# Performance work log

Hardware: AMD Instinct MI355X
Metric: run time of the kernel (lower is better)

The kernel has to match this reference:

```python
import jax, jax.numpy as jnp
import numpy as np

N, G, D, A = 131072, 256, 256, 64
NEG = -1e9
EPS = 1e-10


def segment_softmax(logits, idx, num_segments):
    # numerically stable softmax over ragged segments; works for [N] and [N, A]
    m = jax.ops.segment_max(logits, idx, num_segments=num_segments)
    e = jnp.exp(logits - m[idx])
    s = jax.ops.segment_sum(e, idx, num_segments=num_segments)
    return e / s[idx]


def setup_inputs() -> dict:
    key = jax.random.key(0)
    ks = jax.random.split(key, 12)
    values = jax.random.normal(ks[0], (N, D), dtype=jnp.float32)
    indices = jnp.sort(jax.random.randint(ks[1], (N,), 0, G))
    a_action = jax.random.randint(ks[2], (G,), 0, A)
    a_node = jax.random.randint(ks[3], (G,), 0, N)
    action_mask = jax.random.randint(ks[4], (G, A), 0, 2).astype(bool)
    n_nodes = jax.ops.segment_sum(jnp.ones((N,), jnp.int32), indices, num_segments=G)
    s = 0.02
    w_node = jax.random.normal(ks[5], (D,), dtype=jnp.float32) * s          # node_prob (no bias)
    W_agn = jax.random.normal(ks[6], (A, D), dtype=jnp.float32) * s         # action_given_node_prob
    b_agn = jnp.zeros((A,), jnp.float32)
    W_nga = jax.random.normal(ks[7], (A, D), dtype=jnp.float32) * s         # node_given_action_prob
    b_nga = jnp.zeros((A,), jnp.float32)
    W_qna = jax.random.normal(ks[8], (A, D), dtype=jnp.float32) * s         # q_node__action
    b_qna = jnp.zeros((A,), jnp.float32)
    W_qan = jax.random.normal(ks[9], (A, D), dtype=jnp.float32) * s         # q_action__node
    b_qan = jnp.zeros((A,), jnp.float32)
    return {"values": values, "indices": indices, "a_action": a_action, "a_node": a_node,
            "action_mask": action_mask, "n_nodes": n_nodes,
            "w_node": w_node, "W_agn": W_agn, "b_agn": b_agn, "W_nga": W_nga, "b_nga": b_nga,
            "W_qna": W_qna, "b_qna": b_qna, "W_qan": W_qan, "b_qan": b_qan}


def reference(values, indices, a_action, a_node, action_mask, n_nodes,
              w_node, W_agn, b_agn, W_nga, b_nga, W_qna, b_qna, W_qan, b_qan):
    n_g = action_mask.shape[0]
    segsum = lambda x: jax.ops.segment_sum(x, indices, num_segments=n_g)

    node_logits = values @ w_node                         # [N]
    agn_logits = values @ W_agn.T + b_agn                 # [N, A] action_given_node
    nga_logits = values @ W_nga.T + b_nga                 # [N, A] node_given_action
    mask_actions = action_mask[indices]                   # [N, A] per-node action validity

    # p(n) per graph, p(a|n) per node, p(a) per graph by marginalization
    p_n = segment_softmax(node_logits, indices, n_g)                       # [N]
    p_a_given_n = jax.nn.softmax(jnp.where(mask_actions, agn_logits, NEG), axis=-1)  # [N, A]
    p_a = segsum(p_n[:, None] * p_a_given_n)                               # [G, A]

    # masked p(n|a) used for eval (logprob/entropy)
    p_n_a_masked = segment_softmax(jnp.where(mask_actions, nga_logits, NEG), indices, n_g)  # [N, A]

    g_ar = jnp.arange(n_g)
    logprob = jnp.log(p_a[g_ar, a_action] + EPS) + jnp.log(p_n_a_masked[a_node, a_action] + EPS)  # [G]

    H_a = -jnp.sum(p_a * jnp.log(p_a + EPS), axis=-1)                      # [G]
    H_n_given_a = -segsum(p_n_a_masked * jnp.log(p_n_a_masked + EPS))      # [G, A]
    entropy = H_a + jnp.sum(p_a * H_n_given_a, axis=-1)                    # [G]

    # value estimate (unmasked p_n__a, as in f())
    p_n__a = segment_softmax(nga_logits, indices, n_g)                     # [N, A]
    q_a = segsum(values @ W_qan.T + b_qan)                                 # [G, A]
    q_n__a = values @ W_qna.T + b_qna                                      # [N, A]
    value = jnp.sum(p_a * (q_a + segsum(p_n__a * q_n__a)), axis=-1)        # [G]

    return (logprob, entropy, value, p_a, p_n__a)
```

## Files before the change

### kernel.cpp

```cpp
#include <hip/hip_runtime.h>
#include <hip/hip_bf16.h>

typedef unsigned short u16;
typedef unsigned int u32;
typedef __attribute__((ext_vector_type(4))) float f32x4;
typedef __attribute__((ext_vector_type(8))) short s16x8;
typedef __attribute__((ext_vector_type(8))) unsigned short u16x8;
typedef __attribute__((ext_vector_type(4))) unsigned short u16x4;

#define EPS_V (1e-10f)
#define TILES 4
#define NHALF (TILES * 4)

__device__ __forceinline__ u16 f2bf(float f) {
  unsigned u = __float_as_uint(f);
  u += 0x7fffu + ((u >> 16) & 1u);
  return (u16)(u >> 16);
}
__device__ __forceinline__ float bf2f(u16 h) {
  return __uint_as_float(((unsigned)h) << 16);
}
__device__ __forceinline__ float wred_sum(float v) {
#pragma unroll
  for (int o = 32; o; o >>= 1) v += __shfl_xor(v, o);
  return v;
}
__device__ __forceinline__ bool mask_at(const void* m, int kind, int idx) {
  if (kind == 0) return ((const int*)m)[idx] != 0;
  if (kind == 1) return ((const float*)m)[idx] != 0.0f;
  return ((const unsigned char*)m)[idx] != 0;
}

__global__ __launch_bounds__(256) void k0_fused(
    const int* __restrict__ n_nodes, const unsigned int* __restrict__ mask_raw,
    const float* __restrict__ w_node, const float* __restrict__ W_agn,
    const float* __restrict__ W_nga, const float* __restrict__ W_qna,
    const float* __restrict__ W_qan,
    int* __restrict__ seg_start, int* __restrict__ mkind,
    float* __restrict__ q_a, u16* __restrict__ Wpack, int G, int ndw) {
  const int b = blockIdx.x;
  const int t = threadIdx.x;
  if (b == 0) {
    if (t < 64) {
      int base = t * 4;
      int v0 = (base + 0 < G) ? n_nodes[base + 0] : 0;
      int v1 = (base + 1 < G) ? n_nodes[base + 1] : 0;
      int v2 = (base + 2 < G) ? n_nodes[base + 2] : 0;
      int v3 = (base + 3 < G) ? n_nodes[base + 3] : 0;
      int lsum = v0 + v1 + v2 + v3;
      int x = lsum;
#pragma unroll
      for (int o = 1; o < 64; o <<= 1) {
        int y = __shfl_up(x, o);
        if (t >= o) x += y;
      }
      int run = x - lsum;
      if (base + 0 < G) seg_start[base + 0] = run; run += v0;
      if (base + 1 < G) seg_start[base + 1] = run; run += v1;
      if (base + 2 < G) seg_start[base + 2] = run; run += v2;
      if (base + 3 < G) seg_start[base + 3] = run; run += v3;
      if (t == 63) seg_start[G] = run;
    }
  } else if (b == 1) {
    __shared__ int notInt, notFloat;
    if (t == 0) { notInt = 0; notFloat = 0; }
    __syncthreads();
    int li = 0, lf = 0;
    for (int i = t; i < ndw; i += 256) {
      unsigned v = mask_raw[i];
      if (v != 0u && v != 1u) li = 1;
      if (v != 0u && v != 0x3F800000u) lf = 1;
    }
    if (li) atomicOr(&notInt, 1);
    if (lf) atomicOr(&notFloat, 1);
    __syncthreads();
    if (t == 0) mkind[0] = (!notInt) ? 0 : ((!notFloat) ? 1 : 2);
  } else if (b < 2 + 80) {
    int q = (b - 2) * 256 + t;
    int col = q >> 6, k = (q & 63) * 4;
    f32x4 v = (f32x4){0.f, 0.f, 0.f, 0.f};
    if (col < 64) v = *reinterpret_cast<const f32x4*>(W_agn + col * 256 + k);
    else if (col < 128) v = *reinterpret_cast<const f32x4*>(W_nga + (col - 64) * 256 + k);
    else if (col < 192) v = *reinterpret_cast<const f32x4*>(W_qna + (col - 128) * 256 + k);
    else if (col < 256) v = *reinterpret_cast<const f32x4*>(W_qan + (col - 192) * 256 + k);
    else if (col == 256) v = *reinterpret_cast<const f32x4*>(w_node + k);
    u16x4 h;
    h[0] = f2bf(v[0]); h[1] = f2bf(v[1]); h[2] = f2bf(v[2]); h[3] = f2bf(v[3]);
    *reinterpret_cast<u16x4*>(Wpack + (size_t)q * 4) = h;
  } else {
    int idx = (b - 82) * 256 + t;
    if (idx < G * 64) q_a[idx] = 0.f;
  }
}

__device__ __forceinline__ s16x8 frag_from_lds(const float* Vf, int m, int k0) {
  int g0 = ((k0 >> 2) ^ (m & 7));
  int g1 = g0 ^ 1;
  const f32x4 lo = *reinterpret_cast<const f32x4*>(&Vf[m * 256 + g0 * 4]);
  const f32x4 hi = *reinterpret_cast<const f32x4*>(&Vf[m * 256 + g1 * 4]);
  union { s16x8 v; u32 u[4]; } r;
  r.u[0] = __builtin_amdgcn_perm(__float_as_uint(lo[1]), __float_as_uint(lo[0]), 0x07060302u);
  r.u[1] = __builtin_amdgcn_perm(__float_as_uint(lo[3]), __float_as_uint(lo[2]), 0x07060302u);
  r.u[2] = __builtin_amdgcn_perm(__float_as_uint(hi[1]), __float_as_uint(hi[0]), 0x07060302u);
  r.u[3] = __builtin_amdgcn_perm(__float_as_uint(hi[3]), __float_as_uint(hi[2]), 0x07060302u);
  return r.v;
}

__global__ __launch_bounds__(256, 2) void k1_gemm(
    const float* __restrict__ values, const u16* __restrict__ Wpack,
    const int* __restrict__ indices,
    const float* __restrict__ b_agn, const float* __restrict__ b_nga,
    const float* __restrict__ b_qna, const float* __restrict__ b_qan,
    u16* __restrict__ agn, u16* __restrict__ nga_bf, float* __restrict__ nga_f32,
    u16* __restrict__ qna, float* __restrict__ q_a,
    float* __restrict__ nl, int nga_is_bf) {
  __shared__ float ring[4][16 * 256];
  __shared__ u16 outbuf[3][16][68];
  __shared__ float nlbuf[16];
  __shared__ int segid[TILES * 64];

  const int t = threadIdx.x;
  const int lane = t & 63;
  const int wave = t >> 6;
  const int ln15 = lane & 15;
  const int kg = lane >> 4;
  const int blk0 = blockIdx.x * (TILES * 64);

  s16x8 bfr[4][8];
  {
    const u16* wb = Wpack + (size_t)(wave * 64 + ln15) * 256 + kg * 8;
#pragma unroll
    for (int cg = 0; cg < 4; ++cg)
#pragma unroll
      for (int s = 0; s < 8; ++s)
        bfr[cg][s] = *reinterpret_cast<const s16x8*>(wb + (size_t)(cg * 16) * 256 + s * 32);
  }
  float bias_c[4];
  {
    const float* bp = (wave == 0) ? b_agn : (wave == 1) ? b_nga
                    : (wave == 2) ? b_qna : b_qan;
#pragma unroll
    for (int cg = 0; cg < 4; ++cg) bias_c[cg] = bp[cg * 16 + ln15];
  }
  s16x8 bn[8];
  if (wave == 0) {
    const u16* wb = Wpack + (size_t)(256 + ln15) * 256 + kg * 8;
#pragma unroll
    for (int s = 0; s < 8; ++s)
      bn[s] = *reinterpret_cast<const s16x8*>(wb + s * 32);
  }
  if (wave == 3) {
#pragma unroll
    for (int j = 0; j < 4; ++j)
      segid[lane + 64 * j] = indices[blk0 + lane + 64 * j];
  }
  float qpart[4] = {0.f, 0.f, 0.f, 0.f};
  int qg = (wave == 3) ? segid[kg * 4] : 0;

#define STAGE(hh)                                                              \
  {                                                                            \
    float* dst_ = ring[(hh) & 3];                                              \
    const int r0_ = blk0 + (hh) * 16;                                          \
    _Pragma("unroll")                                                          \
    for (int i_ = 0; i_ < 4; ++i_) {                                           \
      int m_ = wave * 4 + i_;                                                  \
      const float* gp_ = values + (size_t)(r0_ + m_) * 256 + ((lane ^ (m_ & 7)) << 2); \
      __builtin_amdgcn_global_load_lds(                                        \
          (const __attribute__((address_space(1))) void*)gp_,                  \
          (__attribute__((address_space(3))) void*)&dst_[m_ * 256], 16, 0, 0); \
    }                                                                          \
  }

  STAGE(0);
  STAGE(1);

  for (int h = 0; h < NHALF; ++h) {
    if (h + 2 < NHALF) STAGE(h + 2);
    if (!nga_is_bf && wave == 1) {
      asm volatile("s_waitcnt vmcnt(0)" ::: "memory");
    } else if (h == 0) {
      asm volatile("s_waitcnt vmcnt(8)" ::: "memory");
    } else if (h == NHALF - 1) {
      asm volatile("s_waitcnt vmcnt(0)" ::: "memory");
    } else if (h == NHALF - 2) {
      if (wave == 0)      asm volatile("s_waitcnt vmcnt(9)" ::: "memory");
      else if (wave == 3) asm volatile("s_waitcnt vmcnt(4)" ::: "memory");
      else                asm volatile("s_waitcnt vmcnt(8)" ::: "memory");
    } else {
      if (wave == 0)      asm volatile("s_waitcnt vmcnt(13)" ::: "memory");
      else if (wave == 3) asm volatile("s_waitcnt vmcnt(8)" ::: "memory");
      else                asm volatile("s_waitcnt vmcnt(12)" ::: "memory");
    }
    __builtin_amdgcn_sched_barrier(0);
    __builtin_amdgcn_s_barrier();
    __builtin_amdgcn_sched_barrier(0);

    const float* buf = ring[h & 3];
    const int row0 = blk0 + h * 16;

    f32x4 acc[4];
#pragma unroll
    for (int cg = 0; cg < 4; ++cg) acc[cg] = (f32x4){0.f, 0.f, 0.f, 0.f};
    f32x4 an0 = (f32x4){0.f, 0.f, 0.f, 0.f};

#pragma unroll
    for (int s = 0; s < 8; ++s) {
      const int k0 = s * 32 + kg * 8;
      s16x8 a0 = frag_from_lds(buf, ln15, k0);
#pragma unroll
      for (int cg = 0; cg < 4; ++cg)
        acc[cg] = __builtin_amdgcn_mfma_f32_16x16x32_bf16(a0, bfr[cg][s], acc[cg], 0, 0, 0);
      if (wave == 0)
        an0 = __builtin_amdgcn_mfma_f32_16x16x32_bf16(a0, bn[s], an0, 0, 0, 0);
    }

    if (wave == 3) {
#pragma unroll
      for (int r = 0; r < 4; ++r) {
        int m = kg * 4 + r;
        int g = segid[h * 16 + m];
        if (g != qg) {
#pragma unroll
          for (int cg = 0; cg < 4; ++cg) {
            atomicAdd(&q_a[qg * 64 + cg * 16 + ln15], qpart[cg]);
            qpart[cg] = 0.f;
          }
          qg = g;
        }
#pragma unroll
        for (int cg = 0; cg < 4; ++cg)
          qpart[cg] += acc[cg][r] + bias_c[cg];
      }
    } else if (wave == 1 && !nga_is_bf) {
#pragma unroll
      for (int r = 0; r < 4; ++r)
#pragma unroll
        for (int cg = 0; cg < 4; ++cg)
          nga_f32[(size_t)(row0 + kg * 4 + r) * 64 + cg * 16 + ln15] = acc[cg][r] + bias_c[cg];
    } else {
#pragma unroll
      for (int r = 0; r < 4; ++r) {
        int m = kg * 4 + r;
#pragma unroll
        for (int cg = 0; cg < 4; ++cg)
          outbuf[wave][m][cg * 16 + ln15] = f2bf(acc[cg][r] + bias_c[cg]);
      }
      if (wave == 0 && ln15 == 0) {
#pragma unroll
        for (int r = 0; r < 4; ++r) nlbuf[kg * 4 + r] = an0[r];
      }
      u16* dstp = (wave == 0) ? agn : (wave == 1) ? nga_bf : qna;
#pragma unroll
      for (int j = 0; j < 4; ++j) {
        int li = lane + j * 64;
        int rr = li >> 4, cc = (li & 15) * 4;
        u16x4 v = *reinterpret_cast<const u16x4*>(&outbuf[wave][rr][cc]);
        *reinterpret_cast<u16x4*>(dstp + (size_t)row0 * 64 + (size_t)li * 4) = v;
      }
      if (wave == 0 && lane < 16) nl[row0 + lane] = nlbuf[lane];
    }
  }
#undef STAGE

  if (wave == 3) {
#pragma unroll
    for (int cg = 0; cg < 4; ++cg)
      atomicAdd(&q_a[qg * 64 + cg * 16 + ln15], qpart[cg]);
  }
}

__global__ __launch_bounds__(1024) void k2_segment(
    const u16* __restrict__ agn, const u16* __restrict__ nga_bf,
    float* __restrict__ nga_f32, const u16* __restrict__ qna,
    const float* __restrict__ nl, const int* __restrict__ seg_start,
    const void* __restrict__ mask, const int* __restrict__ mkind,
    const float* __restrict__ q_a,
    float* __restrict__ p_a, float* __restrict__ entropy, float* __restrict__ value,
    float* __restrict__ Su, float* __restrict__ pna, int nga_is_bf) {
  const int g = blockIdx.x;
  const int s = seg_start[g], e = seg_start[g + 1];
  const int n = e - s;
  const int t = threadIdx.x, lane = t & 63, wave = t >> 6;

  __shared__ float wbuf[16];
  __shared__ float cs[16][64], cv[16][64], ci[16][64], cp[16][64];
  __shared__ float sS[64];

  float ls = 0.f;
  for (int i = s + t; i < e; i += 1024) ls += __expf(nl[i]);
  ls = wred_sum(ls);
  if (lane == 0) wbuf[wave] = ls;
  __syncthreads();
  float Sn = 0.f;
#pragma unroll
  for (int w = 0; w < 16; ++w) Sn += wbuf[w];
  float invSn = (Sn > 0.f) ? 1.f / Sn : 0.f;

  const int kind = mkind[0];
  const bool mv = mask_at(mask, kind, g * 64 + lane);
  float s_u = 0.f, v_u = 0.f, i_u = 0.f, pa = 0.f;
  for (int i = s + wave; i < e; i += 16) {
    size_t base = (size_t)i * 64 + lane;
    float pn = __expf(nl[i]) * invSn;
    float ev = mv ? __expf(bf2f(agn[base])) : 0.f;
    float rs = wred_sum(ev);
    pa += pn * ((rs > 0.f) ? ev / rs : 0.015625f);
    float y = nga_is_bf ? bf2f(nga_bf[base]) : nga_f32[base];
    float ey = __expf(y);
    s_u += ey;
    v_u += ey * y;
    i_u += ey * bf2f(qna[base]);
  }
  cs[wave][lane] = s_u; cv[wave][lane] = v_u; ci[wave][lane] = i_u;
  cp[wave][lane] = pa;
  __syncthreads();

  if (t < 64) {
    int a = t;
    float S = 0.f, V = 0.f, I = 0.f, P = 0.f;
#pragma unroll
    for (int w = 0; w < 16; ++w) {
      S += cs[w][a]; V += cv[w][a]; I += ci[w][a]; P += cp[w][a];
    }
    p_a[g * 64 + a] = P;
    Su[g * 64 + a] = S;
    sS[a] = (S > 0.f) ? 1.f / S : 0.f;
    float inner = (S > 0.f) ? I / S : 0.f;
    float Q = q_a[g * 64 + a];
    bool mva = mask_at(mask, kind, g * 64 + a);
    float Hn;
    if (n <= 0) Hn = 0.f;
    else if (!mva) Hn = -logf(1.0f / (float)n + EPS_V);
    else Hn = (S > 0.f) ? (logf(S) - V / S) : 0.f;
    float ent_c = -P * logf(P + EPS_V) + P * Hn;
    float val_c = P * (Q + inner);
    ent_c = wred_sum(ent_c);
    val_c = wred_sum(val_c);
    if (a == 0) { entropy[g] = ent_c; value[g] = val_c; }
  }
  __syncthreads();

  const int a0 = (t & 7) * 8;
  float is0 = sS[a0 + 0], is1 = sS[a0 + 1], is2 = sS[a0 + 2], is3 = sS[a0 + 3];
  float is4 = sS[a0 + 4], is5 = sS[a0 + 5], is6 = sS[a0 + 6], is7 = sS[a0 + 7];
  for (int i = s + (t >> 3); i < e; i += 128) {
    size_t base = (size_t)i * 64 + a0;
    float4 o0, o1;
    if (nga_is_bf) {
      u16x8 y = *reinterpret_cast<const u16x8*>(nga_bf + base);
      o0.x = __expf(bf2f(y[0])) * is0; o0.y = __expf(bf2f(y[1])) * is1;
      o0.z = __expf(bf2f(y[2])) * is2; o0.w = __expf(bf2f(y[3])) * is3;
      o1.x = __expf(bf2f(y[4])) * is4; o1.y = __expf(bf2f(y[5])) * is5;
      o1.z = __expf(bf2f(y[6])) * is6; o1.w = __expf(bf2f(y[7])) * is7;
    } else {
      const float4* src = reinterpret_cast<const float4*>(nga_f32 + base);
      float4 x0 = src[0], x1 = src[1];
      o0.x = __expf(x0.x) * is0; o0.y = __expf(x0.y) * is1;
      o0.z = __expf(x0.z) * is2; o0.w = __expf(x0.w) * is3;
      o1.x = __expf(x1.x) * is4; o1.y = __expf(x1.y) * is5;
      o1.z = __expf(x1.z) * is6; o1.w = __expf(x1.w) * is7;
    }
    float4* dst = reinterpret_cast<float4*>(pna + base);
    dst[0] = o0; dst[1] = o1;
  }
}

__global__ __launch_bounds__(256) void k3_logprob(
    const float* __restrict__ p_a, const u16* __restrict__ nga_bf,
    const float* __restrict__ nga_f32, const int* __restrict__ indices,
    const int* __restrict__ a_action, const int* __restrict__ a_node,
    const void* __restrict__ mask, const int* __restrict__ mkind,
    const int* __restrict__ n_nodes, const float* __restrict__ Su,
    float* __restrict__ logprob, int G, int nga_is_bf) {
  int g = blockIdx.x * blockDim.x + threadIdx.x;
  if (g >= G) return;
  int kind = mkind[0];
  int a = a_action[g];
  float t1 = logf(p_a[g * 64 + a] + EPS_V);
  int node = a_node[g];
  int g2 = indices[node];
  float p2;
  if (mask_at(mask, kind, g2 * 64 + a)) {
    float S = Su[g2 * 64 + a];
    float y = nga_is_bf ? bf2f(nga_bf[(size_t)node * 64 + a]) : nga_f32[(size_t)node * 64 + a];
    p2 = (S > 0.f) ? __expf(y) / S : 0.f;
  } else {
    p2 = 1.0f / (float)n_nodes[g2];
  }
  logprob[g] = t1 + logf(p2 + EPS_V);
}

extern "C" void kernel_launch(void* const* d_in, const int* in_sizes, int n_in,
                              void* d_out, int out_size, void* d_ws, size_t ws_size,
                              hipStream_t stream) {
  const float* values = (const float*)d_in[0];
  const int* indices = (const int*)d_in[1];
  const int* a_action = (const int*)d_in[2];
  const int* a_node = (const int*)d_in[3];
  const void* action_mask = d_in[4];
  const int* n_nodes = (const int*)d_in[5];
  const float* w_node = (const float*)d_in[6];
  const float* W_agn = (const float*)d_in[7];
  const float* b_agn = (const float*)d_in[8];
  const float* W_nga = (const float*)d_in[9];
  const float* b_nga = (const float*)d_in[10];
  const float* W_qna = (const float*)d_in[11];
  const float* b_qna = (const float*)d_in[12];
  const float* W_qan = (const float*)d_in[13];
  const float* b_qan = (const float*)d_in[14];

  const int N = in_sizes[1];
  const int G = in_sizes[2];
  const int GA = in_sizes[4];

  float* out = (float*)d_out;
  float* o_logprob = out;
  float* o_entropy = out + G;
  float* o_value = out + 2 * G;
  float* o_pa = out + 3 * G;
  float* o_pna = out + 3 * G + GA;

  char* w = (char*)d_ws;
  size_t off = 0;
  u16* agn = (u16*)(w + off); off += (size_t)N * 64 * 2;
  u16* qna = (u16*)(w + off); off += (size_t)N * 64 * 2;
  float* nl = (float*)(w + off); off += (size_t)N * 4;
  float* Su = (float*)(w + off); off += (size_t)GA * 4;
  float* q_a = (float*)(w + off); off += (size_t)GA * 4;
  int* seg_start = (int*)(w + off); off += (size_t)(G + 1) * 4;
  int* mkind = (int*)(w + off); off += 256;
  off = (off + 255) & ~(size_t)255;
  u16* Wpack = (u16*)(w + off); off += (size_t)320 * 256 * 2;
  u16* nga_bf = (u16*)(w + off);
  size_t need_bf = off + (size_t)N * 64 * 2;
  int nga_is_bf = (ws_size >= need_bf) ? 1 : 0;
  float* nga_f32 = o_pna;

  int zero_blocks = (GA + 255) / 256;
  k0_fused<<<2 + 80 + zero_blocks, 256, 0, stream>>>(
      n_nodes, (const unsigned int*)action_mask, w_node, W_agn, W_nga, W_qna, W_qan,
      seg_start, mkind, q_a, Wpack, G, GA / 4);
  k1_gemm<<<N / (TILES * 64), 256, 0, stream>>>(
      values, Wpack, indices, b_agn, b_nga, b_qna, b_qan,
      agn, nga_bf, nga_f32, qna, q_a, nl, nga_is_bf);
  k2_segment<<<G, 1024, 0, stream>>>(agn, nga_bf, nga_f32, qna, nl, seg_start,
                                     action_mask, mkind, q_a,
                                     o_pa, o_entropy, o_value, Su, o_pna, nga_is_bf);
  k3_logprob<<<(G + 255) / 256, 256, 0, stream>>>(
      o_pa, nga_bf, nga_f32, indices, a_action, a_node,
      action_mask, mkind, n_nodes, Su, o_logprob, G, nga_is_bf);
}
```

Measured before the change: 95.87 us.

## Fuse action-given-node softmax and p_a accumulation into GEMM epilogue

The GEMM kernel now computes the masked per-row softmax of the action-given-node logits, along with the exponentiated node logits, directly in wave 0's epilogue. It accumulates unnormalized p_a and the node-softmax denominator per segment with atomics, so the bf16 agn and nl intermediates are no longer written to or reread from global memory. The segment kernel then only normalizes p_a by the accumulated denominator. This removes about 16MB of intermediate traffic and a reduction pass. The cost is extra exp and shuffle work plus atomics in the GEMM. Node logits are also exponentiated without max subtraction, which relies on them being small.

Measured after the change: 95.52 us (median of 2 runs). About the same (-0.4%).

```diff
diff --git a/kernel.cpp b/kernel.cpp
--- a/kernel.cpp
+++ b/kernel.cpp
@@ -25,6 +25,11 @@
   for (int o = 32; o; o >>= 1) v += __shfl_xor(v, o);
   return v;
 }
+__device__ __forceinline__ float red16(float v) {
+  v += __shfl_xor(v, 1); v += __shfl_xor(v, 2);
+  v += __shfl_xor(v, 4); v += __shfl_xor(v, 8);
+  return v;
+}
 __device__ __forceinline__ bool mask_at(const void* m, int kind, int idx) {
   if (kind == 0) return ((const int*)m)[idx] != 0;
   if (kind == 1) return ((const float*)m)[idx] != 0.0f;
@@ -37,7 +42,8 @@
     const float* __restrict__ W_nga, const float* __restrict__ W_qna,
     const float* __restrict__ W_qan,
     int* __restrict__ seg_start, int* __restrict__ mkind,
-    float* __restrict__ q_a, u16* __restrict__ Wpack, int G, int ndw) {
+    float* __restrict__ zero_base, int nzero, u16* __restrict__ Wpack,
+    int G, int ndw) {
   const int b = blockIdx.x;
   const int t = threadIdx.x;
   if (b == 0) {
@@ -89,7 +95,7 @@
     *reinterpret_cast<u16x4*>(Wpack + (size_t)q * 4) = h;
   } else {
     int idx = (b - 82) * 256 + t;
-    if (idx < G * 64) q_a[idx] = 0.f;
+    if (idx < nzero) zero_base[idx] = 0.f;
   }
 }
 
@@ -108,15 +114,15 @@
 
 __global__ __launch_bounds__(256, 2) void k1_gemm(
     const float* __restrict__ values, const u16* __restrict__ Wpack,
-    const int* __restrict__ indices,
+    const int* __restrict__ indices, const void* __restrict__ mask,
+    const int* __restrict__ mkind,
     const float* __restrict__ b_agn, const float* __restrict__ b_nga,
     const float* __restrict__ b_qna, const float* __restrict__ b_qan,
-    u16* __restrict__ agn, u16* __restrict__ nga_bf, float* __restrict__ nga_f32,
+    u16* __restrict__ nga_bf, float* __restrict__ nga_f32,
     u16* __restrict__ qna, float* __restrict__ q_a,
-    float* __restrict__ nl, int nga_is_bf) {
+    float* __restrict__ pa_un, float* __restrict__ Sn_at, int nga_is_bf) {
   __shared__ float ring[4][16 * 256];
-  __shared__ u16 outbuf[3][16][68];
-  __shared__ float nlbuf[16];
+  __shared__ u16 outbuf[2][16][68];
   __shared__ int segid[TILES * 64];
 
   const int t = threadIdx.x;
@@ -125,6 +131,7 @@
   const int ln15 = lane & 15;
   const int kg = lane >> 4;
   const int blk0 = blockIdx.x * (TILES * 64);
+  const int kind = mkind[0];
 
   s16x8 bfr[4][8];
   {
@@ -156,6 +163,16 @@
   }
   float qpart[4] = {0.f, 0.f, 0.f, 0.f};
   int qg = (wave == 3) ? segid[kg * 4] : 0;
+  float pa_[4] = {0.f, 0.f, 0.f, 0.f};
+  float sn_ = 0.f;
+  int pg = 0;
+  bool mv[4] = {false, false, false, false};
+  if (wave == 0) {
+    pg = indices[blk0 + kg * 4];
+#pragma unroll
+    for (int cg = 0; cg < 4; ++cg)
+      mv[cg] = mask_at(mask, kind, pg * 64 + cg * 16 + ln15);
+  }
 
 #define STAGE(hh)                                                              \
   {                                                                            \
@@ -176,20 +193,18 @@
 
   for (int h = 0; h < NHALF; ++h) {
     if (h + 2 < NHALF) STAGE(h + 2);
-    if (!nga_is_bf && wave == 1) {
+    if (h == 0) {
+      asm volatile("s_waitcnt vmcnt(8) lgkmcnt(0)" ::: "memory");
+    } else if (!nga_is_bf && wave == 1) {
       asm volatile("s_waitcnt vmcnt(0)" ::: "memory");
-    } else if (h == 0) {
-      asm volatile("s_waitcnt vmcnt(8)" ::: "memory");
     } else if (h == NHALF - 1) {
       asm volatile("s_waitcnt vmcnt(0)" ::: "memory");
     } else if (h == NHALF - 2) {
-      if (wave == 0)      asm volatile("s_waitcnt vmcnt(9)" ::: "memory");
-      else if (wave == 3) asm volatile("s_waitcnt vmcnt(4)" ::: "memory");
-      else                asm volatile("s_waitcnt vmcnt(8)" ::: "memory");
+      if (wave == 1 || wave == 2) asm volatile("s_waitcnt vmcnt(8)" ::: "memory");
+      else                        asm volatile("s_waitcnt vmcnt(4)" ::: "memory");
     } else {
-      if (wave == 0)      asm volatile("s_waitcnt vmcnt(13)" ::: "memory");
-      else if (wave == 3) asm volatile("s_waitcnt vmcnt(8)" ::: "memory");
-      else                asm volatile("s_waitcnt vmcnt(12)" ::: "memory");
+      if (wave == 1 || wave == 2) asm volatile("s_waitcnt vmcnt(12)" ::: "memory");
+      else                        asm volatile("s_waitcnt vmcnt(8)" ::: "memory");
     }
     __builtin_amdgcn_sched_barrier(0);
     __builtin_amdgcn_s_barrier();
@@ -214,7 +229,44 @@
         an0 = __builtin_amdgcn_mfma_f32_16x16x32_bf16(a0, bn[s], an0, 0, 0, 0);
     }
 
-    if (wave == 3) {
+    if (wave == 0) {
+#pragma unroll
+      for (int r = 0; r < 4; ++r) {
+        int m = kg * 4 + r;
+        int g = segid[h * 16 + m];
+        if (g != pg) {
+#pragma unroll
+          for (int cg = 0; cg < 4; ++cg) {
+            atomicAdd(&pa_un[pg * 64 + cg * 16 + ln15], pa_[cg]);
+            pa_[cg] = 0.f;
+          }
+          if (ln15 == 0) atomicAdd(&Sn_at[pg], sn_);
+          sn_ = 0.f;
+          pg = g;
+#pragma unroll
+          for (int cg = 0; cg < 4; ++cg)
+            mv[cg] = mask_at(mask, kind, pg * 64 + cg * 16 + ln15);
+        }
+        float e0[4];
+        float rs = 0.f;
+#pragma unroll
+        for (int cg = 0; cg < 4; ++cg) {
+          e0[cg] = mv[cg] ? __expf(acc[cg][r] + bias_c[cg]) : 0.f;
+          rs += e0[cg];
+        }
+        rs = red16(rs);
+        float pn_e = __shfl(__expf(an0[r]), kg * 16);
+        if (ln15 == 0) sn_ += pn_e;
+        if (rs > 0.f) {
+          float inv = pn_e / rs;
+#pragma unroll
+          for (int cg = 0; cg < 4; ++cg) pa_[cg] += e0[cg] * inv;
+        } else {
+#pragma unroll
+          for (int cg = 0; cg < 4; ++cg) pa_[cg] += pn_e * 0.015625f;
+        }
+      }
+    } else if (wave == 3) {
 #pragma unroll
       for (int r = 0; r < 4; ++r) {
         int m = kg * 4 + r;
@@ -243,21 +295,16 @@
         int m = kg * 4 + r;
 #pragma unroll
         for (int cg = 0; cg < 4; ++cg)
-          outbuf[wave][m][cg * 16 + ln15] = f2bf(acc[cg][r] + bias_c[cg]);
+          outbuf[wave - 1][m][cg * 16 + ln15] = f2bf(acc[cg][r] + bias_c[cg]);
       }
-      if (wave == 0 && ln15 == 0) {
-#pragma unroll
-        for (int r = 0; r < 4; ++r) nlbuf[kg * 4 + r] = an0[r];
-      }
-      u16* dstp = (wave == 0) ? agn : (wave == 1) ? nga_bf : qna;
+      u16* dstp = (wave == 1) ? nga_bf : qna;
 #pragma unroll
       for (int j = 0; j < 4; ++j) {
         int li = lane + j * 64;
         int rr = li >> 4, cc = (li & 15) * 4;
-        u16x4 v = *reinterpret_cast<const u16x4*>(&outbuf[wave][rr][cc]);
+        u16x4 v = *reinterpret_cast<const u16x4*>(&outbuf[wave - 1][rr][cc]);
         *reinterpret_cast<u16x4*>(dstp + (size_t)row0 * 64 + (size_t)li * 4) = v;
       }
-      if (wave == 0 && lane < 16) nl[row0 + lane] = nlbuf[lane];
     }
   }
 #undef STAGE
@@ -267,14 +314,20 @@
     for (int cg = 0; cg < 4; ++cg)
       atomicAdd(&q_a[qg * 64 + cg * 16 + ln15], qpart[cg]);
   }
+  if (wave == 0) {
+#pragma unroll
+    for (int cg = 0; cg < 4; ++cg)
+      atomicAdd(&pa_un[pg * 64 + cg * 16 + ln15], pa_[cg]);
+    if (ln15 == 0) atomicAdd(&Sn_at[pg], sn_);
+  }
 }
 
 __global__ __launch_bounds__(1024) void k2_segment(
-    const u16* __restrict__ agn, const u16* __restrict__ nga_bf,
-    float* __restrict__ nga_f32, const u16* __restrict__ qna,
-    const float* __restrict__ nl, const int* __restrict__ seg_start,
+    const u16* __restrict__ nga_bf, float* __restrict__ nga_f32,
+    const u16* __restrict__ qna, const int* __restrict__ seg_start,
     const void* __restrict__ mask, const int* __restrict__ mkind,
-    const float* __restrict__ q_a,
+    const float* __restrict__ q_a, const float* __restrict__ pa_un,
+    const float* __restrict__ Sn_at,
     float* __restrict__ p_a, float* __restrict__ entropy, float* __restrict__ value,
     float* __restrict__ Su, float* __restrict__ pna, int nga_is_bf) {
   const int g = blockIdx.x;
@@ -282,29 +335,12 @@
   const int n = e - s;
   const int t = threadIdx.x, lane = t & 63, wave = t >> 6;
 
-  __shared__ float wbuf[16];
-  __shared__ float cs[16][64], cv[16][64], ci[16][64], cp[16][64];
+  __shared__ float cs[16][64], cv[16][64], ci[16][64];
   __shared__ float sS[64];
 
-  float ls = 0.f;
-  for (int i = s + t; i < e; i += 1024) ls += __expf(nl[i]);
-  ls = wred_sum(ls);
-  if (lane == 0) wbuf[wave] = ls;
-  __syncthreads();
-  float Sn = 0.f;
-#pragma unroll
-  for (int w = 0; w < 16; ++w) Sn += wbuf[w];
-  float invSn = (Sn > 0.f) ? 1.f / Sn : 0.f;
-
-  const int kind = mkind[0];
-  const bool mv = mask_at(mask, kind, g * 64 + lane);
-  float s_u = 0.f, v_u = 0.f, i_u = 0.f, pa = 0.f;
+  float s_u = 0.f, v_u = 0.f, i_u = 0.f;
   for (int i = s + wave; i < e; i += 16) {
     size_t base = (size_t)i * 64 + lane;
-    float pn = __expf(nl[i]) * invSn;
-    float ev = mv ? __expf(bf2f(agn[base])) : 0.f;
-    float rs = wred_sum(ev);
-    pa += pn * ((rs > 0.f) ? ev / rs : 0.015625f);
     float y = nga_is_bf ? bf2f(nga_bf[base]) : nga_f32[base];
     float ey = __expf(y);
     s_u += ey;
@@ -312,16 +348,16 @@
     i_u += ey * bf2f(qna[base]);
   }
   cs[wave][lane] = s_u; cv[wave][lane] = v_u; ci[wave][lane] = i_u;
-  cp[wave][lane] = pa;
   __syncthreads();
 
+  const int kind = mkind[0];
   if (t < 64) {
     int a = t;
-    float S = 0.f, V = 0.f, I = 0.f, P = 0.f;
-#pragma unroll
-    for (int w = 0; w < 16; ++w) {
-      S += cs[w][a]; V += cv[w][a]; I += ci[w][a]; P += cp[w][a];
-    }
+    float S = 0.f, V = 0.f, I = 0.f;
+#pragma unroll
+    for (int w = 0; w < 16; ++w) { S += cs[w][a]; V += cv[w][a]; I += ci[w][a]; }
+    float Sn = Sn_at[g];
+    float P = (Sn > 0.f) ? pa_un[g * 64 + a] / Sn : 0.f;
     p_a[g * 64 + a] = P;
     Su[g * 64 + a] = S;
     sS[a] = (S > 0.f) ? 1.f / S : 0.f;
@@ -422,11 +458,13 @@
 
   char* w = (char*)d_ws;
   size_t off = 0;
-  u16* agn = (u16*)(w + off); off += (size_t)N * 64 * 2;
   u16* qna = (u16*)(w + off); off += (size_t)N * 64 * 2;
-  float* nl = (float*)(w + off); off += (size_t)N * 4;
   float* Su = (float*)(w + off); off += (size_t)GA * 4;
+  float* zero_base = (float*)(w + off);
   float* q_a = (float*)(w + off); off += (size_t)GA * 4;
+  float* pa_un = (float*)(w + off); off += (size_t)GA * 4;
+  float* Sn_at = (float*)(w + off); off += (size_t)G * 4;
+  int nzero = 2 * GA + G;
   int* seg_start = (int*)(w + off); off += (size_t)(G + 1) * 4;
   int* mkind = (int*)(w + off); off += 256;
   off = (off + 255) & ~(size_t)255;
@@ -436,15 +474,16 @@
   int nga_is_bf = (ws_size >= need_bf) ? 1 : 0;
   float* nga_f32 = o_pna;
 
-  int zero_blocks = (GA + 255) / 256;
+  int zero_blocks = (nzero + 255) / 256;
   k0_fused<<<2 + 80 + zero_blocks, 256, 0, stream>>>(
       n_nodes, (const unsigned int*)action_mask, w_node, W_agn, W_nga, W_qna, W_qan,
-      seg_start, mkind, q_a, Wpack, G, GA / 4);
+      seg_start, mkind, zero_base, nzero, Wpack, G, GA / 4);
   k1_gemm<<<N / (TILES * 64), 256, 0, stream>>>(
-      values, Wpack, indices, b_agn, b_nga, b_qna, b_qan,
-      agn, nga_bf, nga_f32, qna, q_a, nl, nga_is_bf);
-  k2_segment<<<G, 1024, 0, stream>>>(agn, nga_bf, nga_f32, qna, nl, seg_start,
-                                     action_mask, mkind, q_a,
+      values, Wpack, indices, action_mask, mkind,
+      b_agn, b_nga, b_qna, b_qan,
+      nga_bf, nga_f32, qna, q_a, pa_un, Sn_at, nga_is_bf);
+  k2_segment<<<G, 1024, 0, stream>>>(nga_bf, nga_f32, qna, seg_start,
+                                     action_mask, mkind, q_a, pa_un, Sn_at,
                                      o_pa, o_entropy, o_value, Su, o_pna, nga_is_bf);
   k3_logprob<<<(G + 255) / 256, 256, 0, stream>>>(
       o_pa, nga_bf, nga_f32, indices, a_action, a_node,
```
